# Kernel optimization log

Hardware: AMD Instinct MI355X
Metric: run time of the kernel (lower is better)

## Reference

```python
import jax, jax.numpy as jnp
import numpy as np

DIM = 2048
N_HEADS = 32
N_KV_HEADS = 8
HEAD_DIM = DIM // N_HEADS
B, T = 2, 2048


def setup_inputs() -> dict:
    key = jax.random.key(0)
    ks = jax.random.split(key, 5)
    std = 0.02
    return {
        "x": jax.random.normal(ks[0], (B, T, DIM), dtype=jnp.float32),
        "wq": jax.random.normal(ks[1], (DIM, DIM), dtype=jnp.float32) * std,
        "wk": jax.random.normal(ks[2], (N_KV_HEADS * HEAD_DIM, DIM), dtype=jnp.float32) * std,
        "wv": jax.random.normal(ks[3], (N_KV_HEADS * HEAD_DIM, DIM), dtype=jnp.float32) * std,
        "wo": jax.random.normal(ks[4], (DIM, DIM), dtype=jnp.float32) * std,
    }


def _rope_tables(seq_len, head_dim, dtype):
    inv_freq = 1.0 / (10000.0 ** (jnp.arange(0, head_dim, 2, dtype=jnp.float32) / head_dim))
    t = jnp.arange(seq_len, dtype=jnp.float32)
    freqs = jnp.einsum("i,j->ij", t, inv_freq)          # [T, hd/2]
    emb = jnp.concatenate([freqs, freqs], axis=-1)       # [T, hd]
    return jnp.cos(emb).astype(dtype), jnp.sin(emb).astype(dtype)


def _rotate_half(x):
    h = x.shape[-1] // 2
    return jnp.concatenate([-x[..., h:], x[..., :h]], axis=-1)


def reference(x, wq, wk, wv, wo):
    Bc, Tc, C = x.shape
    q = (x @ wq.T).reshape(Bc, Tc, N_HEADS, HEAD_DIM).transpose(0, 2, 1, 3)      # [B,H,T,hd]
    k = (x @ wk.T).reshape(Bc, Tc, N_KV_HEADS, HEAD_DIM).transpose(0, 2, 1, 3)   # [B,Hk,T,hd]
    v = (x @ wv.T).reshape(Bc, Tc, N_KV_HEADS, HEAD_DIM).transpose(0, 2, 1, 3)

    cos, sin = _rope_tables(Tc, HEAD_DIM, x.dtype)  # [T,hd] broadcast over B,H
    q = q * cos + _rotate_half(q) * sin
    k = k * cos + _rotate_half(k) * sin

    rep = N_HEADS // N_KV_HEADS
    k = jnp.repeat(k, rep, axis=1)  # [B,H,T,hd]
    v = jnp.repeat(v, rep, axis=1)

    scale = 1.0 / np.sqrt(HEAD_DIM)
    scores = jnp.einsum("bhqd,bhkd->bhqk", q, k) * scale   # [B,H,T,T]
    causal = jnp.triu(jnp.ones((Tc, Tc), dtype=bool), k=1)
    scores = jnp.where(causal, jnp.asarray(-jnp.inf, scores.dtype), scores)
    attn = jax.nn.softmax(scores, axis=-1)
    out = jnp.einsum("bhqk,bhkd->bhqd", attn, v)           # [B,H,T,hd]
    out = out.transpose(0, 2, 1, 3).reshape(Bc, Tc, C)
    return out @ wo.T
```

## Files before the change

### kernel.cpp

```cpp
#include <hip/hip_runtime.h>


typedef unsigned short u16;
typedef __attribute__((ext_vector_type(8))) short bf16x8;
typedef __attribute__((ext_vector_type(4))) float f32x4;
typedef __attribute__((ext_vector_type(4))) unsigned short u16x4;

constexpr int T_SEQ = 2048;
constexpr int DIMC  = 2048;
constexpr int NHEAD = 32;
constexpr int HDIM  = 64;
constexpr int KVDIM = 512;
constexpr int BATCH = 2;

__device__ __forceinline__ u16 f2bf(float f) {
    union { float f; unsigned int i; } v; v.f = f;
    unsigned int r = v.i + 0x7FFFu + ((v.i >> 16) & 1u);
    return (u16)(r >> 16);
}

__device__ __forceinline__ unsigned int pack2_bf16(float e0, float e1) {
    return __builtin_amdgcn_perm(__float_as_uint(e1), __float_as_uint(e0),
                                 0x07060302u);
}

typedef __attribute__((address_space(1))) unsigned int as1_uint;
typedef __attribute__((address_space(3))) unsigned int as3_uint;
__device__ __forceinline__ void glds16(const u16* g, u16* l) {
    __builtin_amdgcn_global_load_lds((as1_uint*)(u16*)g, (as3_uint*)l, 16, 0, 0);
}

__global__ __launch_bounds__(256) void cvt5(const float* __restrict__ x,
                                            const float* __restrict__ wq,
                                            const float* __restrict__ wk,
                                            const float* __restrict__ wv,
                                            const float* __restrict__ wo,
                                            u16* __restrict__ xb,  u16* __restrict__ wqb,
                                            u16* __restrict__ wkb, u16* __restrict__ wvb,
                                            u16* __restrict__ wob) {
    constexpr int E0 = BATCH * T_SEQ * DIMC;
    constexpr int E1 = E0 + DIMC * DIMC;
    constexpr int E2 = E1 + KVDIM * DIMC;
    constexpr int E3 = E2 + KVDIM * DIMC;
    constexpr int E4 = E3 + DIMC * DIMC;
    for (int i = (blockIdx.x * 256 + threadIdx.x) * 4; i < E4; i += gridDim.x * 1024) {
        const float* s; u16* d; int off;
        if (i < E0)      { s = x;  d = xb;  off = 0;  }
        else if (i < E1) { s = wq; d = wqb; off = E0; }
        else if (i < E2) { s = wk; d = wkb; off = E1; }
        else if (i < E3) { s = wv; d = wvb; off = E2; }
        else             { s = wo; d = wob; off = E3; }
        f32x4 v = *(const f32x4*)(s + (i - off));
        u16x4 o;
        #pragma unroll
        for (int e = 0; e < 4; ++e) o[e] = f2bf(v[e]);
        *(u16x4*)(d + (i - off)) = o;
    }
}

template <bool OUTF32>
__device__ __forceinline__ void dgemm_core(const u16* __restrict__ A,
                                           const u16* __restrict__ W,
                                           void* __restrict__ Cv,
                                           int rowBase, int colBase,
                                           int N, int K, bool rope) {
    __shared__ __align__(16) u16 Ash[2][128 * 64];
    __shared__ __align__(16) u16 Bsh[2][128 * 64];

    const int tid  = threadIdx.x;
    const int lane = tid & 63;
    const int w    = tid >> 6;
    const int quad = lane >> 4;
    const int ln   = lane & 15;
    const int wm   = (w >> 1) * 64;
    const int wn   = (w & 1) * 64;

    const int sr = lane >> 3;
    const int sc = 8 * ((lane & 7) ^ sr);
    const u16* aS = A + (size_t)(rowBase + w * 8 + sr) * K + sc;
    const u16* bS = W + (size_t)(colBase + w * 8 + sr) * K + sc;

    f32x4 acc[4][4] = {};
    const int NT = K / 64;

    #pragma unroll
    for (int r = 0; r < 4; ++r) {
        glds16(aS + (size_t)(r * 32) * K, &Ash[0][(w + 4 * r) * 512]);
        glds16(bS + (size_t)(r * 32) * K, &Bsh[0][(w + 4 * r) * 512]);
    }

    for (int t = 0; t < NT; ++t) {
        const int cb = t & 1;
        __builtin_amdgcn_s_barrier();
        __builtin_amdgcn_sched_barrier(0);

        if (t + 1 < NT) {
            const size_t ko = (size_t)(t + 1) * 64;
            u16* An = &Ash[cb ^ 1][0];
            u16* Bn = &Bsh[cb ^ 1][0];
            #pragma unroll
            for (int r = 0; r < 4; ++r) {
                glds16(aS + ko + (size_t)(r * 32) * K, An + (w + 4 * r) * 512);
                glds16(bS + ko + (size_t)(r * 32) * K, Bn + (w + 4 * r) * 512);
            }
            __builtin_amdgcn_sched_barrier(0);
            __asm__ __volatile__("s_waitcnt vmcnt(8)" ::: "memory");
        } else {
            __asm__ __volatile__("s_waitcnt vmcnt(0)" ::: "memory");
        }
        __builtin_amdgcn_sched_barrier(0);
        __builtin_amdgcn_s_barrier();

        const u16* Ap = &Ash[cb][0];
        const u16* Bp = &Bsh[cb][0];
        const int swz = (ln & 7) * 8;
        #pragma unroll
        for (int q2 = 0; q2 < 2; ++q2) {
            bf16x8 bwf[4];
            #pragma unroll
            for (int n = 0; n < 4; ++n)
                bwf[n] = *(const bf16x8*)(Bp + (wn + n * 16 + ln) * 64
                                             + ((q2 * 32 + quad * 8) ^ swz));
            __builtin_amdgcn_s_setprio(1);
            #pragma unroll
            for (int m = 0; m < 4; ++m) {
                bf16x8 af = *(const bf16x8*)(Ap + (wm + m * 16 + ln) * 64
                                                + ((q2 * 32 + quad * 8) ^ swz));
                #pragma unroll
                for (int n = 0; n < 4; ++n)
                    acc[m][n] = __builtin_amdgcn_mfma_f32_16x16x32_bf16(af, bwf[n], acc[m][n], 0, 0, 0);
            }
            __builtin_amdgcn_s_setprio(0);
        }
    }

    if (rope) {
        #pragma unroll
        for (int j = 0; j < 2; ++j) {
            const int d = j * 16 + ln;
            const float invrev = exp2f(-(float)d * (13.287712379549449f / 32.0f))
                                 * 0.15915494309189535f;
            #pragma unroll
            for (int i = 0; i < 4; ++i) {
                #pragma unroll
                for (int r = 0; r < 4; ++r) {
                    const int t = (rowBase + wm + i * 16 + quad * 4 + r) & (T_SEQ - 1);
                    float rev = (float)t * invrev;
                    float fr = rev - floorf(rev);
                    float sn = __builtin_amdgcn_sinf(fr);
                    float cs = __builtin_amdgcn_cosf(fr);
                    float a0 = acc[i][j][r], a2 = acc[i][j + 2][r];
                    acc[i][j][r]     = a0 * cs - a2 * sn;
                    acc[i][j + 2][r] = a2 * cs + a0 * sn;
                }
            }
        }
    }

    #pragma unroll
    for (int i = 0; i < 4; ++i) {
        int mrow = rowBase + wm + i * 16 + quad * 4;
        #pragma unroll
        for (int j = 0; j < 4; ++j) {
            int n = colBase + wn + j * 16 + ln;
            #pragma unroll
            for (int r = 0; r < 4; ++r) {
                if constexpr (OUTF32)
                    ((float*)Cv)[(size_t)(mrow + r) * N + n] = acc[i][j][r];
                else
                    ((u16*)Cv)[(size_t)(mrow + r) * N + n] = f2bf(acc[i][j][r]);
            }
        }
    }
}

__global__ __launch_bounds__(256, 2) void qkv_gemm(const u16* __restrict__ xb,
                                                   const u16* __restrict__ wqb,
                                                   const u16* __restrict__ wkb,
                                                   const u16* __restrict__ wvb,
                                                   u16* __restrict__ Qb,
                                                   u16* __restrict__ Kb,
                                                   u16* __restrict__ Vb) {
    const int flat = blockIdx.y * 24 + blockIdx.x;
    const int nf   = (flat & 7) * 96 + (flat >> 3);
    const int ct   = nf % 24;
    const int rowBase = (nf / 24) * 128;

    const u16* W; u16* C; int colBase, N; bool rope;
    if (ct < 16)      { W = wqb; C = Qb; colBase = ct * 128;        N = DIMC;  rope = true; }
    else if (ct < 20) { W = wkb; C = Kb; colBase = (ct - 16) * 128; N = KVDIM; rope = true; }
    else              { W = wvb; C = Vb; colBase = (ct - 20) * 128; N = KVDIM; rope = false; }
    dgemm_core<false>(xb, W, C, rowBase, colBase, N, DIMC, rope);
}

__global__ __launch_bounds__(256, 2) void gemm_out(const u16* __restrict__ A,
                                                   const u16* __restrict__ W,
                                                   float* __restrict__ C) {
    const int flat = blockIdx.y * 16 + blockIdx.x;
    const int nf   = (flat & 7) * 64 + (flat >> 3);
    const int colBase = (nf % 16) * 128;
    const int rowBase = (nf / 16) * 128;
    dgemm_core<true>(A, W, C, rowBase, colBase, DIMC, DIMC, false);
}

__global__ __launch_bounds__(256) void transpose_v(const u16* __restrict__ V,
                                                   u16* __restrict__ Vt) {
    __shared__ __align__(16) u16 tile[32][33];
    const int x = threadIdx.x & 31;
    const int y = threadIdx.x >> 5;
    const int tok0 = blockIdx.y * 32;
    const int c0   = blockIdx.x * 32;
    #pragma unroll
    for (int yy = 0; yy < 32; yy += 8)
        tile[y + yy][x] = V[(size_t)(tok0 + y + yy) * KVDIM + c0 + x];
    __syncthreads();
    const int b  = tok0 >> 11;
    const int t0 = tok0 & (T_SEQ - 1);
    #pragma unroll
    for (int yy = 0; yy < 32; yy += 8)
        Vt[(size_t)(b * KVDIM + c0 + y + yy) * T_SEQ + t0 + x] = tile[x][y + yy];
}

__global__ __launch_bounds__(256) void attn(const u16* __restrict__ Q,
                                            const u16* __restrict__ Kx,
                                            const u16* __restrict__ Vt,
                                            u16* __restrict__ O) {
    __shared__ __align__(16) u16 Ks[2][64][72];
    __shared__ __align__(16) u16 Vs[2][64][72];

    const int tid  = threadIdx.x;
    const int lane = tid & 63;
    const int w    = tid >> 6;
    const int quad = lane >> 4;
    const int ln   = lane & 15;
    const int h    = blockIdx.y;
    const int b    = blockIdx.z;
    const int kvh  = h >> 2;

    const int srow = tid >> 2;
    const int c    = tid & 3;
    const int scol = c * 16;
    const int vsb  = 32 * (c >> 1) + 4 * (c & 1);
    const u16* kbase = Kx + (size_t)(b * T_SEQ + srow) * KVDIM + kvh * HDIM + scol;
    const u16* vbase = Vt + (size_t)(b * KVDIM + kvh * HDIM + srow) * T_SEQ;

    const float K1 = 0.125f * 1.4426950408889634f;
    const float K2 = 8.0f * 1.4426950408889634f;

    #pragma unroll
    for (int phase = 0; phase < 2; ++phase) {
        const int qt = phase ? (31 - (int)blockIdx.x) : (int)blockIdx.x;
        const int qr0 = qt * 64 + w * 16;

        const u16* qp = Q + (size_t)(b * T_SEQ + qr0 + ln) * DIMC + h * HDIM + quad * 8;
        const bf16x8 bq0 = *(const bf16x8*)qp;
        const bf16x8 bq1 = *(const bf16x8*)(qp + 32);

        f32x4 o[4] = {};
        float lsum = 0.0f;

        bf16x8 kra = *(const bf16x8*)kbase;
        bf16x8 krb = *(const bf16x8*)(kbase + 8);
        bf16x8 vra = *(const bf16x8*)(vbase + scol);
        bf16x8 vrb = *(const bf16x8*)(vbase + scol + 8);

        for (int kt = 0; kt <= qt; ++kt) {
            const int cb = kt & 1;

            *(bf16x8*)&Ks[cb][srow][scol]     = kra;
            *(bf16x8*)&Ks[cb][srow][scol + 8] = krb;
            {
                union { bf16x8 v; u16x4 h4[2]; } ua, ub;
                ua.v = vra; ub.v = vrb;
                *(u16x4*)&Vs[cb][srow][vsb]      = ua.h4[0];
                *(u16x4*)&Vs[cb][srow][vsb + 8]  = ua.h4[1];
                *(u16x4*)&Vs[cb][srow][vsb + 16] = ub.h4[0];
                *(u16x4*)&Vs[cb][srow][vsb + 24] = ub.h4[1];
            }

            if (kt < qt) {
                const size_t ko = (size_t)(kt + 1) * 64;
                kra = *(const bf16x8*)(kbase + ko * KVDIM);
                krb = *(const bf16x8*)(kbase + ko * KVDIM + 8);
                vra = *(const bf16x8*)(vbase + ko + scol);
                vrb = *(const bf16x8*)(vbase + ko + scol + 8);
            }

            __asm__ __volatile__("s_waitcnt lgkmcnt(0)" ::: "memory");
            __builtin_amdgcn_s_barrier();

            f32x4 s[4];
            __builtin_amdgcn_s_setprio(1);
            #pragma unroll
            for (int st = 0; st < 4; ++st) {
                f32x4 z = {};
                s[st] = __builtin_amdgcn_mfma_f32_16x16x32_bf16(
                            *(const bf16x8*)&Ks[cb][st * 16 + ln][quad * 8], bq0, z, 0, 0, 0);
                s[st] = __builtin_amdgcn_mfma_f32_16x16x32_bf16(
                            *(const bf16x8*)&Ks[cb][st * 16 + ln][32 + quad * 8], bq1, s[st], 0, 0, 0);
            }
            __builtin_amdgcn_s_setprio(0);

            unsigned int pk[8];
            if (kt != qt) {
                #pragma unroll
                for (int st = 0; st < 4; ++st) {
                    float e0 = exp2f(fmaf(s[st][0], K1, -K2));
                    float e1 = exp2f(fmaf(s[st][1], K1, -K2));
                    float e2 = exp2f(fmaf(s[st][2], K1, -K2));
                    float e3 = exp2f(fmaf(s[st][3], K1, -K2));
                    lsum += (e0 + e1) + (e2 + e3);
                    pk[2 * st]     = pack2_bf16(e0, e1);
                    pk[2 * st + 1] = pack2_bf16(e2, e3);
                }
            } else {
                const int thr = w * 16 + ln;
                #pragma unroll
                for (int st = 0; st < 4; ++st) {
                    float e[4];
                    #pragma unroll
                    for (int r = 0; r < 4; ++r) {
                        const int key = st * 16 + quad * 4 + r;
                        e[r] = (key > thr) ? 0.0f : exp2f(fmaf(s[st][r], K1, -K2));
                    }
                    lsum += (e[0] + e[1]) + (e[2] + e[3]);
                    pk[2 * st]     = pack2_bf16(e[0], e[1]);
                    pk[2 * st + 1] = pack2_bf16(e[2], e[3]);
                }
            }

            union { unsigned int u[4]; bf16x8 v; } a0, a1;
            a0.u[0] = pk[0]; a0.u[1] = pk[1]; a0.u[2] = pk[2]; a0.u[3] = pk[3];
            a1.u[0] = pk[4]; a1.u[1] = pk[5]; a1.u[2] = pk[6]; a1.u[3] = pk[7];

            __builtin_amdgcn_s_setprio(1);
            #pragma unroll
            for (int t = 0; t < 4; ++t) {
                o[t] = __builtin_amdgcn_mfma_f32_16x16x32_bf16(
                           a0.v, *(const bf16x8*)&Vs[cb][t * 16 + ln][quad * 8], o[t], 0, 0, 0);
                o[t] = __builtin_amdgcn_mfma_f32_16x16x32_bf16(
                           a1.v, *(const bf16x8*)&Vs[cb][t * 16 + ln][32 + quad * 8], o[t], 0, 0, 0);
            }
            __builtin_amdgcn_s_setprio(0);
        }

        float ls = lsum;
        ls += __shfl_xor(ls, 16);
        ls += __shfl_xor(ls, 32);
        #pragma unroll
        for (int r = 0; r < 4; ++r) {
            const float inv = 1.0f / __shfl(ls, quad * 4 + r);
            size_t obase = (size_t)(b * T_SEQ + qr0 + quad * 4 + r) * DIMC + h * HDIM;
            #pragma unroll
            for (int t = 0; t < 4; ++t)
                O[obase + t * 16 + ln] = f2bf(o[t][r] * inv);
        }

        __syncthreads();
    }
}

extern "C" void kernel_launch(void* const* d_in, const int* in_sizes, int n_in,
                              void* d_out, int out_size, void* d_ws, size_t ws_size,
                              hipStream_t stream) {
    const float* x  = (const float*)d_in[0];
    const float* wq = (const float*)d_in[1];
    const float* wk = (const float*)d_in[2];
    const float* wv = (const float*)d_in[3];
    const float* wo = (const float*)d_in[4];
    float* out = (float*)d_out;

    char* ws = (char*)d_ws;
    constexpr size_t MB = 1024 * 1024;
    u16* Qb  = (u16*)(ws);
    u16* Kb  = (u16*)(ws + 16 * MB);
    u16* Vb  = (u16*)(ws + 20 * MB);
    u16* Vtb = (u16*)(ws + 24 * MB);
    u16* AOb = (u16*)(ws + 28 * MB);
    u16* xb  = AOb;
    u16* wqb = (u16*)(ws + 44 * MB);
    u16* wkb = (u16*)(ws + 52 * MB);
    u16* wvb = (u16*)(ws + 54 * MB);
    u16* wob = (u16*)(ws + 56 * MB);
    const int M = BATCH * T_SEQ;

    hipLaunchKernelGGL(cvt5, dim3(2048), dim3(256), 0, stream,
                       x, wq, wk, wv, wo, xb, wqb, wkb, wvb, wob);
    hipLaunchKernelGGL(qkv_gemm, dim3(24, M / 128), dim3(256), 0, stream,
                       xb, wqb, wkb, wvb, Qb, Kb, Vb);
    hipLaunchKernelGGL(transpose_v, dim3(KVDIM / 32, M / 32), dim3(256), 0, stream, Vb, Vtb);
    hipLaunchKernelGGL(attn, dim3(16, NHEAD, BATCH), dim3(256), 0, stream,
                       Qb, Kb, Vtb, AOb);
    hipLaunchKernelGGL(gemm_out, dim3(DIMC / 128, M / 128), dim3(256), 0, stream,
                       AOb, wob, out);
}
```

Before: 288.8 us.

## Load GEMM weight fragments directly into registers instead of staging through LDS

The weight (B) operand of the bf16 GEMM core is no longer staged in shared memory. Each lane now loads its MFMA B fragments straight from global memory into double-buffered registers one tile ahead, and the loop is unrolled by two so it can alternate between the buffers. This halves LDS usage and removes the B LDS writes and reads, which could raise occupancy and cut LDS traffic. In exchange it adds register pressure and issues uncoalesced 16-byte global loads, and the B data is no longer shared across the waves that use the same columns. The unroll-by-two also assumes NT is even.

```diff
diff --git a/kernel.cpp b/kernel.cpp
--- a/kernel.cpp
+++ b/kernel.cpp
@@ -65,7 +65,6 @@
                                            int rowBase, int colBase,
                                            int N, int K, bool rope) {
     __shared__ __align__(16) u16 Ash[2][128 * 64];
-    __shared__ __align__(16) u16 Bsh[2][128 * 64];
 
     const int tid  = threadIdx.x;
     const int lane = tid & 63;
@@ -78,60 +77,64 @@
     const int sr = lane >> 3;
     const int sc = 8 * ((lane & 7) ^ sr);
     const u16* aS = A + (size_t)(rowBase + w * 8 + sr) * K + sc;
-    const u16* bS = W + (size_t)(colBase + w * 8 + sr) * K + sc;
+
+    const u16* bP = W + (size_t)(colBase + wn + ln) * K + quad * 8;
 
     f32x4 acc[4][4] = {};
     const int NT = K / 64;
-
-    #pragma unroll
-    for (int r = 0; r < 4; ++r) {
+    const int swz = (ln & 7) * 8;
+
+    #pragma unroll
+    for (int r = 0; r < 4; ++r)
         glds16(aS + (size_t)(r * 32) * K, &Ash[0][(w + 4 * r) * 512]);
-        glds16(bS + (size_t)(r * 32) * K, &Bsh[0][(w + 4 * r) * 512]);
-    }
-
-    for (int t = 0; t < NT; ++t) {
-        const int cb = t & 1;
+    bf16x8 bA[8], bB[8];
+    #pragma unroll
+    for (int n = 0; n < 4; ++n) {
+        bA[2 * n]     = *(const bf16x8*)(bP + (size_t)(n * 16) * K);
+        bA[2 * n + 1] = *(const bf16x8*)(bP + (size_t)(n * 16) * K + 32);
+    }
+
+    auto tile_step = [&](int t, u16* Abuf, u16* Anext, bf16x8* bc, bf16x8* bn) {
         __builtin_amdgcn_s_barrier();
         __builtin_amdgcn_sched_barrier(0);
-
         if (t + 1 < NT) {
             const size_t ko = (size_t)(t + 1) * 64;
-            u16* An = &Ash[cb ^ 1][0];
-            u16* Bn = &Bsh[cb ^ 1][0];
-            #pragma unroll
-            for (int r = 0; r < 4; ++r) {
-                glds16(aS + ko + (size_t)(r * 32) * K, An + (w + 4 * r) * 512);
-                glds16(bS + ko + (size_t)(r * 32) * K, Bn + (w + 4 * r) * 512);
-            }
+            #pragma unroll
+            for (int r = 0; r < 4; ++r)
+                glds16(aS + ko + (size_t)(r * 32) * K, Anext + (w + 4 * r) * 512);
             __builtin_amdgcn_sched_barrier(0);
-            __asm__ __volatile__("s_waitcnt vmcnt(8)" ::: "memory");
+            __asm__ __volatile__("s_waitcnt vmcnt(4)" ::: "memory");
+            __builtin_amdgcn_sched_barrier(0);
+            #pragma unroll
+            for (int n = 0; n < 4; ++n) {
+                bn[2 * n]     = *(const bf16x8*)(bP + (size_t)(n * 16) * K + ko);
+                bn[2 * n + 1] = *(const bf16x8*)(bP + (size_t)(n * 16) * K + ko + 32);
+            }
+            __builtin_amdgcn_sched_barrier(0);
         } else {
             __asm__ __volatile__("s_waitcnt vmcnt(0)" ::: "memory");
-        }
-        __builtin_amdgcn_sched_barrier(0);
+            __builtin_amdgcn_sched_barrier(0);
+        }
         __builtin_amdgcn_s_barrier();
-
-        const u16* Ap = &Ash[cb][0];
-        const u16* Bp = &Bsh[cb][0];
-        const int swz = (ln & 7) * 8;
         #pragma unroll
         for (int q2 = 0; q2 < 2; ++q2) {
-            bf16x8 bwf[4];
-            #pragma unroll
-            for (int n = 0; n < 4; ++n)
-                bwf[n] = *(const bf16x8*)(Bp + (wn + n * 16 + ln) * 64
-                                             + ((q2 * 32 + quad * 8) ^ swz));
             __builtin_amdgcn_s_setprio(1);
             #pragma unroll
             for (int m = 0; m < 4; ++m) {
-                bf16x8 af = *(const bf16x8*)(Ap + (wm + m * 16 + ln) * 64
-                                                + ((q2 * 32 + quad * 8) ^ swz));
+                bf16x8 af = *(const bf16x8*)(Abuf + (wm + m * 16 + ln) * 64
+                                                  + ((q2 * 32 + quad * 8) ^ swz));
                 #pragma unroll
                 for (int n = 0; n < 4; ++n)
-                    acc[m][n] = __builtin_amdgcn_mfma_f32_16x16x32_bf16(af, bwf[n], acc[m][n], 0, 0, 0);
+                    acc[m][n] = __builtin_amdgcn_mfma_f32_16x16x32_bf16(
+                                    af, bc[2 * n + q2], acc[m][n], 0, 0, 0);
             }
             __builtin_amdgcn_s_setprio(0);
         }
+    };
+
+    for (int t = 0; t < NT; t += 2) {
+        tile_step(t,     &Ash[0][0], &Ash[1][0], bA, bB);
+        tile_step(t + 1, &Ash[1][0], &Ash[0][0], bB, bA);
     }
 
     if (rope) {
```

Result: slower. 364.4 us (+26.2%).
